# Performance work log

Measured on AMD Instinct MI355X. Metric: run time of the kernel, lower is better.

The kernel has to match this reference:

```python
import jax, jax.numpy as jnp
import numpy as np

TOPK = 6
ROUTE_SCALE = 1.5


def setup_inputs() -> dict:
    key = jax.random.key(0)
    k1, k2, k3 = jax.random.split(key, 3)
    N, D, E = 16384, 4096, 256
    x = jax.random.normal(k1, (N, D), dtype=jnp.float32)
    weight = jax.random.normal(k2, (E, D), dtype=jnp.float32) * (D ** -0.5)
    bias = jax.random.normal(k3, (E,), dtype=jnp.float32) * 0.02
    return {"x": x, "weight": weight, "bias": bias}


def reference(x, weight, bias):
    # gate linear: [N, D] @ [E, D]^T -> [N, E], computed in fp32
    scores = jnp.einsum('nd,ed->ne', x.astype(jnp.float32), weight.astype(jnp.float32))
    # sqrtsoftplus score function
    original_scores = jnp.sqrt(jax.nn.softplus(scores))
    # bias only affects expert selection, not the routing weights
    biased = original_scores + bias
    _, indices = jax.lax.top_k(biased, TOPK)          # [N, TOPK] int32
    weights = jnp.take_along_axis(original_scores, indices, axis=-1)
    # non-softmax score func -> renormalize selected weights
    weights = weights / jnp.sum(weights, axis=-1, keepdims=True)
    weights = weights * ROUTE_SCALE
    return weights, indices
```

## Files before the change

### kernel.cpp

```cpp
#include <hip/hip_runtime.h>
#include <math.h>

constexpr int D     = 4096;
constexpr int D4    = 1024;
constexpr int E     = 256;
constexpr int TK    = 6;
constexpr int BM    = 64;
constexpr int NT    = 512;
constexpr int NTILE = 128;
constexpr float TAU = 3e-5f;

typedef __attribute__((ext_vector_type(8)))  short short8;
typedef __attribute__((ext_vector_type(16))) float float16;
typedef unsigned short ushort_t;

#define GAS __attribute__((address_space(1)))
#define LAS __attribute__((address_space(3)))

__device__ __forceinline__ ushort_t f2bf(float f) {
  unsigned u = __float_as_uint(f);
  return (ushort_t)((u + 0x7fffu + ((u >> 16) & 1u)) >> 16);
}
__device__ __forceinline__ float bf2f(ushort_t h) {
  return __uint_as_float(((unsigned)h) << 16);
}
__device__ __forceinline__ int swz4(int r) { return (r & 3) ^ ((r >> 2) & 3); }

__device__ __forceinline__ void gload_lds16(const ushort_t* g, ushort_t* l) {
  __builtin_amdgcn_global_load_lds((const GAS unsigned int*)g,
                                   (LAS unsigned int*)l, 16, 0, 0);
}

struct __align__(16) SMem {
  union {
    struct {
      ushort_t Bh[4][8][32 * 32];
      ushort_t Bl[4][8][32 * 32];
      ushort_t Ah[2][BM * 32];
      ushort_t Al[2][BM * 32];
    } st;
    struct {
      float val[BM * 65];
      int   id [BM * 65];
    } mg;
  } u;
  float  bias[E];
  int    nflag;
  int    flagrow[BM];
  int    flagid[BM][8];
  double exact[8];
};
static_assert(sizeof(SMem) <= 160 * 1024, "LDS overflow");

__global__ __launch_bounds__(256)
void conv_w(const float* __restrict__ wg, ushort_t* __restrict__ whi,
            ushort_t* __restrict__ wlo)
{
  size_t i = (size_t)blockIdx.x * 256 + threadIdx.x;
  float4 v = ((const float4*)wg)[i];
  float a[4] = {v.x, v.y, v.z, v.w};
  ushort_t h[4], l[4];
#pragma unroll
  for (int j = 0; j < 4; ++j) {
    h[j] = f2bf(a[j]);
    l[j] = f2bf(a[j] - bf2f(h[j]));
  }
  *(uint2*)&whi[i * 4] = *(uint2*)h;
  *(uint2*)&wlo[i * 4] = *(uint2*)l;
}

#define WAITV5   asm volatile("s_waitcnt vmcnt(5)" ::: "memory")
#define WAITV0   asm volatile("s_waitcnt vmcnt(0)" ::: "memory")
#define LGKM0    asm volatile("s_waitcnt lgkmcnt(0)" ::: "memory")
#define MEMFENCE asm volatile("" ::: "memory")

__global__ __launch_bounds__(NT, 2)
void gate_kernel(const float* __restrict__ xg, const float* __restrict__ wg,
                 const float* __restrict__ bg,
                 const ushort_t* __restrict__ whi, const ushort_t* __restrict__ wlo,
                 float* __restrict__ outw, float* __restrict__ outi)
{
  __shared__ SMem sm;
  const int t    = threadIdx.x;
  const int row0 = blockIdx.x * BM;
  const int wv   = t >> 6;
  const int lane = t & 63;
  const int m    = lane & 31;
  const int hf   = lane >> 5;

  if (t < E) sm.bias[t] = bg[t];
  if (t == 0) sm.nflag = 0;

  const float4* x4 = (const float4*)xg;
  const float4* w4 = (const float4*)wg;

  float16 acc0, acc1;
#pragma unroll
  for (int i = 0; i < 16; ++i) { acc0[i] = 0.f; acc1[i] = 0.f; }

  const int a_row = t >> 3;
  const int a_c   = t & 7;

  const int e16 = lane >> 2;
  const int ch  = lane & 3;

  const int sA = swz4(m);

  auto stage_B = [&](int kt, int p) {
#pragma unroll
    for (int j = 0; j < 2; ++j) {
      const int er = j * 16 + e16;
      const int cs = ch ^ swz4(er);
      const size_t go = (size_t)(wv * 32 + er) * D + kt * 32 + cs * 8;
      gload_lds16(whi + go, &sm.u.st.Bh[p][wv][j * 512]);
      gload_lds16(wlo + go, &sm.u.st.Bl[p][wv][j * 512]);
    }
  };
  auto store_A = [&](int p, float4 xv) {
    float av[4] = {xv.x, xv.y, xv.z, xv.w};
    ushort_t h[4], l[4];
#pragma unroll
    for (int i = 0; i < 4; ++i) {
      h[i] = f2bf(av[i]);
      l[i] = f2bf(av[i] - bf2f(h[i]));
    }
    const int c  = a_c >> 1, hh = a_c & 1;
    const int sl = (c ^ swz4(a_row)) * 8 + hh * 4;
    *(uint2*)&sm.u.st.Ah[p][a_row * 32 + sl] = *(uint2*)h;
    *(uint2*)&sm.u.st.Al[p][a_row * 32 + sl] = *(uint2*)l;
  };
  auto compute = [&](int pa, int pb) {
#pragma unroll
    for (int ks = 0; ks < 2; ++ks) {
      const int sl = ((2 * ks + hf) ^ sA) * 8;
      short8 a0h = *(const short8*)&sm.u.st.Ah[pa][m * 32 + sl];
      short8 a0l = *(const short8*)&sm.u.st.Al[pa][m * 32 + sl];
      short8 a1h = *(const short8*)&sm.u.st.Ah[pa][(32 + m) * 32 + sl];
      short8 a1l = *(const short8*)&sm.u.st.Al[pa][(32 + m) * 32 + sl];
      short8 bh  = *(const short8*)&sm.u.st.Bh[pb][wv][m * 32 + sl];
      short8 bl  = *(const short8*)&sm.u.st.Bl[pb][wv][m * 32 + sl];
      acc0 = __builtin_amdgcn_mfma_f32_32x32x16_bf16(a0h, bh, acc0, 0, 0, 0);
      acc0 = __builtin_amdgcn_mfma_f32_32x32x16_bf16(a0h, bl, acc0, 0, 0, 0);
      acc0 = __builtin_amdgcn_mfma_f32_32x32x16_bf16(a0l, bh, acc0, 0, 0, 0);
      acc1 = __builtin_amdgcn_mfma_f32_32x32x16_bf16(a1h, bh, acc1, 0, 0, 0);
      acc1 = __builtin_amdgcn_mfma_f32_32x32x16_bf16(a1h, bl, acc1, 0, 0, 0);
      acc1 = __builtin_amdgcn_mfma_f32_32x32x16_bf16(a1l, bh, acc1, 0, 0, 0);
    }
  };

  float4 x0 = x4[(size_t)(row0 + a_row) * D4 + 0 * 8 + a_c];
  float4 xA = x4[(size_t)(row0 + a_row) * D4 + 1 * 8 + a_c];
  stage_B(0, 0);
  WAITV5;
  store_A(0, x0);
  float4 xB = x4[(size_t)(row0 + a_row) * D4 + 2 * 8 + a_c];
  stage_B(1, 1);
  LGKM0;
  __builtin_amdgcn_s_barrier();
  MEMFENCE;

#define TILE_BODY(KT, XS)                                                     \
  do {                                                                        \
    const int P   = (KT) & 3;                                                 \
    const int PW  = ((KT) + 2) & 3;                                           \
    const int PA  = (KT) & 1;                                                 \
    const int PA1 = ((KT) + 1) & 1;                                           \
    WAITV5;                                  \
    store_A(PA1, XS);                                                         \
    { const int kl = ((KT) + 3 < NTILE) ? (KT) + 3 : NTILE - 1;               \
      XS = x4[(size_t)(row0 + a_row) * D4 + kl * 8 + a_c]; }                  \
    { const int kb = ((KT) + 2 < NTILE) ? (KT) + 2 : NTILE - 1;               \
      stage_B(kb, PW); }                                                      \
    compute(PA, P);                                                           \
    LGKM0;                          \
    __builtin_amdgcn_s_barrier();                                             \
    MEMFENCE;                                                                 \
  } while (0)

  for (int it = 0; it < NTILE / 4; ++it) {
    const int kt = it * 4;
    TILE_BODY(kt + 0, xA);
    TILE_BODY(kt + 1, xB);
    TILE_BODY(kt + 2, xA);
    TILE_BODY(kt + 3, xB);
  }
#undef TILE_BODY

  WAITV0;
  __syncthreads();

  const int eBase  = wv * 32;
  const int myE    = eBase + m;
  const float myBias = sm.bias[myE];

#pragma unroll
  for (int b = 0; b < 2; ++b) {
#pragma unroll
    for (int reg = 0; reg < 16; ++reg) {
      const int row_local = b * 32 + (reg & 3) + 8 * (reg >> 2) + 4 * hf;
      float s = b ? acc1[reg] : acc0[reg];
      float v = sqrtf(fmaxf(s, 0.f) + log1pf(expf(-fabsf(s)))) + myBias;
#pragma unroll
      for (int ssel = 0; ssel < 8; ++ssel) {
        float bv = v;
#pragma unroll
        for (int off = 1; off < 32; off <<= 1)
          bv = fmaxf(bv, __shfl_xor(bv, off, 64));
        unsigned long long ball = __ballot(v == bv);
        unsigned hm = (unsigned)(ball >> (hf * 32));
        int mwin = __ffs(hm) - 1;
        if (m == mwin) {
          sm.u.mg.val[row_local * 65 + wv * 8 + ssel] = v;
          sm.u.mg.id [row_local * 65 + wv * 8 + ssel] = myE;
          v = -INFINITY;
        }
      }
    }
  }
  __syncthreads();

  {
    const int r = t >> 3, g = t & 7;
    float mv[8]; int mi[8];
#pragma unroll
    for (int q = 0; q < 8; ++q) {
      mv[q] = sm.u.mg.val[r * 65 + q * 8 + g];
      mi[q] = sm.u.mg.id [r * 65 + q * 8 + g];
    }
    float tv[8]; int ti[8];
#pragma unroll
    for (int s = 0; s < 8; ++s) {
      float bv = mv[0]; int bi = mi[0];
#pragma unroll
      for (int q = 1; q < 8; ++q)
        if (mv[q] > bv || (mv[q] == bv && mi[q] < bi)) { bv = mv[q]; bi = mi[q]; }
#pragma unroll
      for (int off = 1; off < 8; off <<= 1) {
        float ov = __shfl_xor(bv, off, 64);
        int   oi = __shfl_xor(bi, off, 64);
        if (ov > bv || (ov == bv && oi < bi)) { bv = ov; bi = oi; }
      }
      tv[s] = bv; ti[s] = bi;
#pragma unroll
      for (int q = 0; q < 8; ++q)
        if (mi[q] == bi) mv[q] = -INFINITY;
    }
    if (g == 0) {
      bool flag = false;
#pragma unroll
      for (int i = 0; i < 7; ++i) flag |= (tv[i] - tv[i + 1] < TAU);
      const int grow = row0 + r;
      if (!flag) {
        float og[6], ssum = 0.f;
#pragma unroll
        for (int i = 0; i < 6; ++i) { og[i] = tv[i] - sm.bias[ti[i]]; ssum += og[i]; }
        const float sc = 1.5f / ssum;
#pragma unroll
        for (int i = 0; i < 6; ++i) {
          outw[(size_t)grow * TK + i] = og[i] * sc;
          outi[(size_t)grow * TK + i] = (float)ti[i];
        }
      } else {
        int slot = atomicAdd(&sm.nflag, 1);
        sm.flagrow[slot] = grow;
#pragma unroll
        for (int i = 0; i < 8; ++i) sm.flagid[slot][i] = ti[i];
      }
    }
  }
  __syncthreads();

  const int nf = sm.nflag;
  for (int f = 0; f < nf; ++f) {
    const int grow = sm.flagrow[f];
    const int e    = sm.flagid[f][wv];
    double accd = 0.0;
    const float4* xr = x4 + (size_t)grow * D4 + lane * 16;
    const float4* wr = w4 + (size_t)e    * D4 + lane * 16;
#pragma unroll
    for (int i = 0; i < 16; ++i) {
      float4 xv = xr[i], wl = wr[i];
      accd = fma((double)xv.x, (double)wl.x, accd);
      accd = fma((double)xv.y, (double)wl.y, accd);
      accd = fma((double)xv.z, (double)wl.z, accd);
      accd = fma((double)xv.w, (double)wl.w, accd);
    }
#pragma unroll
    for (int off = 1; off < 64; off <<= 1)
      accd += __shfl_xor(accd, off, 64);
    if (lane == 0) {
      double sp = fmax(accd, 0.0) + log1p(exp(-fabs(accd)));
      sm.exact[wv] = sqrt(sp);
    }
    __syncthreads();
    if (t == 0) {
      double ov[8]; int oid[8], ordr[8];
      for (int i = 0; i < 8; ++i) { ov[i] = sm.exact[i]; oid[i] = sm.flagid[f][i]; ordr[i] = i; }
      for (int i = 0; i < 6; ++i) {
        int b = i;
        for (int j = i + 1; j < 8; ++j) {
          double bj = ov[ordr[j]] + (double)sm.bias[oid[ordr[j]]];
          double bb = ov[ordr[b]] + (double)sm.bias[oid[ordr[b]]];
          if (bj > bb || (bj == bb && oid[ordr[j]] < oid[ordr[b]])) b = j;
        }
        int tmp = ordr[i]; ordr[i] = ordr[b]; ordr[b] = tmp;
      }
      double ssum = 0.0;
      for (int i = 0; i < 6; ++i) ssum += ov[ordr[i]];
      double sc = 1.5 / ssum;
      for (int i = 0; i < 6; ++i) {
        outw[(size_t)grow * TK + i] = (float)(ov[ordr[i]] * sc);
        outi[(size_t)grow * TK + i] = (float)oid[ordr[i]];
      }
    }
    __syncthreads();
  }
}

extern "C" void kernel_launch(void* const* d_in, const int* in_sizes, int n_in,
                              void* d_out, int out_size, void* d_ws, size_t ws_size,
                              hipStream_t stream) {
  const float* x = (const float*)d_in[0];
  const float* w = (const float*)d_in[1];
  const float* b = (const float*)d_in[2];
  float* out  = (float*)d_out;
  const int N = in_sizes[0] / D;

  ushort_t* whi = (ushort_t*)d_ws;
  ushort_t* wlo = whi + (size_t)E * D;

  float* outw = out;
  float* outi = out + (size_t)N * TK;

  hipLaunchKernelGGL(conv_w, dim3(E * D / 4 / 256), dim3(256), 0, stream,
                     w, whi, wlo);
  hipLaunchKernelGGL(gate_kernel, dim3(N / BM), dim3(NT), 0, stream,
                     x, w, b, whi, wlo, outw, outi);
}
```

Before: 561.8 us.

## Split K across wave pairs with 1024-thread blocks and LDS reduction

Doubles the block to 16 waves. Each pair of waves shares one 32-expert slice and splits the K dimension of each 32-wide tile, one wave per half, instead of one wave walking the full tile. Each wave now stages only the hi or lo weight plane, and loads x as float2 to match the new thread count. Partial accumulators are summed through an LDS reduction buffer before the unchanged top-k epilogue, which runs on half of the waves. The aim is more waves in flight per CU to hide latency, at the cost of extra LDS traffic, a reduction step, idle waves in the epilogue, and stricter register limits from launch_bounds(1024,4).

```diff
diff --git a/kernel.cpp b/kernel.cpp
--- a/kernel.cpp
+++ b/kernel.cpp
@@ -2,11 +2,12 @@
 #include <math.h>
 
 constexpr int D     = 4096;
+constexpr int D2    = 2048;
 constexpr int D4    = 1024;
 constexpr int E     = 256;
 constexpr int TK    = 6;
 constexpr int BM    = 64;
-constexpr int NT    = 512;
+constexpr int NT    = 1024;
 constexpr int NTILE = 128;
 constexpr float TAU = 3e-5f;
 
@@ -40,9 +41,10 @@
       ushort_t Al[2][BM * 32];
     } st;
     struct {
+      float red[8][2][16][64];
       float val[BM * 65];
       int   id [BM * 65];
-    } mg;
+    } ep;
   } u;
   float  bias[E];
   int    nflag;
@@ -69,12 +71,13 @@
   *(uint2*)&wlo[i * 4] = *(uint2*)l;
 }
 
-#define WAITV5   asm volatile("s_waitcnt vmcnt(5)" ::: "memory")
+#define WAITV3   asm volatile("s_waitcnt vmcnt(3)" ::: "memory")
+#define WAITV2   asm volatile("s_waitcnt vmcnt(2)" ::: "memory")
 #define WAITV0   asm volatile("s_waitcnt vmcnt(0)" ::: "memory")
 #define LGKM0    asm volatile("s_waitcnt lgkmcnt(0)" ::: "memory")
 #define MEMFENCE asm volatile("" ::: "memory")
 
-__global__ __launch_bounds__(NT, 2)
+__global__ __launch_bounds__(NT, 4)
 void gate_kernel(const float* __restrict__ xg, const float* __restrict__ wg,
                  const float* __restrict__ bg,
                  const ushort_t* __restrict__ whi, const ushort_t* __restrict__ wlo,
@@ -87,10 +90,13 @@
   const int lane = t & 63;
   const int m    = lane & 31;
   const int hf   = lane >> 5;
+  const int eg   = wv >> 1;
+  const int kh   = wv & 1;
 
   if (t < E) sm.bias[t] = bg[t];
   if (t == 0) sm.nflag = 0;
 
+  const float2* x2 = (const float2*)xg;
   const float4* x4 = (const float4*)xg;
   const float4* w4 = (const float4*)wg;
 
@@ -98,81 +104,76 @@
 #pragma unroll
   for (int i = 0; i < 16; ++i) { acc0[i] = 0.f; acc1[i] = 0.f; }
 
-  const int a_row = t >> 3;
-  const int a_c   = t & 7;
+  const int a_row = t >> 4;
+  const int aq    = t & 15;
 
   const int e16 = lane >> 2;
   const int ch  = lane & 3;
 
   const int sA = swz4(m);
+  const int slR = ((2 * kh + hf) ^ sA) * 8;
+
+  const ushort_t* wsrc = kh ? wlo : whi;
 
   auto stage_B = [&](int kt, int p) {
+    ushort_t* dstbase = kh ? &sm.u.st.Bl[p][eg][0] : &sm.u.st.Bh[p][eg][0];
 #pragma unroll
     for (int j = 0; j < 2; ++j) {
       const int er = j * 16 + e16;
       const int cs = ch ^ swz4(er);
-      const size_t go = (size_t)(wv * 32 + er) * D + kt * 32 + cs * 8;
-      gload_lds16(whi + go, &sm.u.st.Bh[p][wv][j * 512]);
-      gload_lds16(wlo + go, &sm.u.st.Bl[p][wv][j * 512]);
+      const size_t go = (size_t)(eg * 32 + er) * D + kt * 32 + cs * 8;
+      gload_lds16(wsrc + go, dstbase + j * 512);
     }
   };
-  auto store_A = [&](int p, float4 xv) {
-    float av[4] = {xv.x, xv.y, xv.z, xv.w};
-    ushort_t h[4], l[4];
-#pragma unroll
-    for (int i = 0; i < 4; ++i) {
-      h[i] = f2bf(av[i]);
-      l[i] = f2bf(av[i] - bf2f(h[i]));
-    }
-    const int c  = a_c >> 1, hh = a_c & 1;
-    const int sl = (c ^ swz4(a_row)) * 8 + hh * 4;
-    *(uint2*)&sm.u.st.Ah[p][a_row * 32 + sl] = *(uint2*)h;
-    *(uint2*)&sm.u.st.Al[p][a_row * 32 + sl] = *(uint2*)l;
+  auto ldx = [&](int kt) {
+    return x2[(size_t)(row0 + a_row) * D2 + kt * 16 + aq];
+  };
+  auto store_A = [&](int p, float2 xv) {
+    ushort_t h0 = f2bf(xv.x), h1 = f2bf(xv.y);
+    ushort_t l0 = f2bf(xv.x - bf2f(h0)), l1 = f2bf(xv.y - bf2f(h1));
+    const int c = aq >> 2, sub = aq & 3;
+    const int sl = ((c ^ swz4(a_row)) << 3) + sub * 2;
+    unsigned hp = (unsigned)h0 | ((unsigned)h1 << 16);
+    unsigned lp = (unsigned)l0 | ((unsigned)l1 << 16);
+    *(unsigned*)&sm.u.st.Ah[p][a_row * 32 + sl] = hp;
+    *(unsigned*)&sm.u.st.Al[p][a_row * 32 + sl] = lp;
   };
   auto compute = [&](int pa, int pb) {
-#pragma unroll
-    for (int ks = 0; ks < 2; ++ks) {
-      const int sl = ((2 * ks + hf) ^ sA) * 8;
-      short8 a0h = *(const short8*)&sm.u.st.Ah[pa][m * 32 + sl];
-      short8 a0l = *(const short8*)&sm.u.st.Al[pa][m * 32 + sl];
-      short8 a1h = *(const short8*)&sm.u.st.Ah[pa][(32 + m) * 32 + sl];
-      short8 a1l = *(const short8*)&sm.u.st.Al[pa][(32 + m) * 32 + sl];
-      short8 bh  = *(const short8*)&sm.u.st.Bh[pb][wv][m * 32 + sl];
-      short8 bl  = *(const short8*)&sm.u.st.Bl[pb][wv][m * 32 + sl];
-      acc0 = __builtin_amdgcn_mfma_f32_32x32x16_bf16(a0h, bh, acc0, 0, 0, 0);
-      acc0 = __builtin_amdgcn_mfma_f32_32x32x16_bf16(a0h, bl, acc0, 0, 0, 0);
-      acc0 = __builtin_amdgcn_mfma_f32_32x32x16_bf16(a0l, bh, acc0, 0, 0, 0);
-      acc1 = __builtin_amdgcn_mfma_f32_32x32x16_bf16(a1h, bh, acc1, 0, 0, 0);
-      acc1 = __builtin_amdgcn_mfma_f32_32x32x16_bf16(a1h, bl, acc1, 0, 0, 0);
-      acc1 = __builtin_amdgcn_mfma_f32_32x32x16_bf16(a1l, bh, acc1, 0, 0, 0);
-    }
+    short8 a0h = *(const short8*)&sm.u.st.Ah[pa][m * 32 + slR];
+    short8 a0l = *(const short8*)&sm.u.st.Al[pa][m * 32 + slR];
+    short8 a1h = *(const short8*)&sm.u.st.Ah[pa][(32 + m) * 32 + slR];
+    short8 a1l = *(const short8*)&sm.u.st.Al[pa][(32 + m) * 32 + slR];
+    short8 bh  = *(const short8*)&sm.u.st.Bh[pb][eg][m * 32 + slR];
+    short8 bl  = *(const short8*)&sm.u.st.Bl[pb][eg][m * 32 + slR];
+    acc0 = __builtin_amdgcn_mfma_f32_32x32x16_bf16(a0h, bh, acc0, 0, 0, 0);
+    acc0 = __builtin_amdgcn_mfma_f32_32x32x16_bf16(a0h, bl, acc0, 0, 0, 0);
+    acc0 = __builtin_amdgcn_mfma_f32_32x32x16_bf16(a0l, bh, acc0, 0, 0, 0);
+    acc1 = __builtin_amdgcn_mfma_f32_32x32x16_bf16(a1h, bh, acc1, 0, 0, 0);
+    acc1 = __builtin_amdgcn_mfma_f32_32x32x16_bf16(a1h, bl, acc1, 0, 0, 0);
+    acc1 = __builtin_amdgcn_mfma_f32_32x32x16_bf16(a1l, bh, acc1, 0, 0, 0);
   };
 
-  float4 x0 = x4[(size_t)(row0 + a_row) * D4 + 0 * 8 + a_c];
-  float4 xA = x4[(size_t)(row0 + a_row) * D4 + 1 * 8 + a_c];
   stage_B(0, 0);
-  WAITV5;
-  store_A(0, x0);
-  float4 xB = x4[(size_t)(row0 + a_row) * D4 + 2 * 8 + a_c];
   stage_B(1, 1);
+  float2 x0v = ldx(0);
+  float2 xA  = ldx(1);
+  float2 xB  = ldx(2);
+  WAITV2;
+  store_A(0, x0v);
   LGKM0;
   __builtin_amdgcn_s_barrier();
   MEMFENCE;
 
 #define TILE_BODY(KT, XS)                                                     \
   do {                                                                        \
-    const int P   = (KT) & 3;                                                 \
-    const int PW  = ((KT) + 2) & 3;                                           \
-    const int PA  = (KT) & 1;                                                 \
-    const int PA1 = ((KT) + 1) & 1;                                           \
-    WAITV5;                                  \
-    store_A(PA1, XS);                                                         \
+    store_A(((KT) + 1) & 1, XS);                                              \
     { const int kl = ((KT) + 3 < NTILE) ? (KT) + 3 : NTILE - 1;               \
-      XS = x4[(size_t)(row0 + a_row) * D4 + kl * 8 + a_c]; }                  \
+      XS = ldx(kl); }                                                         \
     { const int kb = ((KT) + 2 < NTILE) ? (KT) + 2 : NTILE - 1;               \
-      stage_B(kb, PW); }                                                      \
-    compute(PA, P);                                                           \
-    LGKM0;                          \
+      stage_B(kb, ((KT) + 2) & 3); }                                          \
+    compute((KT) & 1, (KT) & 3);                                              \
+    WAITV3;                                      \
+    LGKM0;                                              \
     __builtin_amdgcn_s_barrier();                                             \
     MEMFENCE;                                                                 \
   } while (0)
@@ -189,43 +190,60 @@
   WAITV0;
   __syncthreads();
 
-  const int eBase  = wv * 32;
-  const int myE    = eBase + m;
+  if (kh == 1) {
+#pragma unroll
+    for (int r = 0; r < 16; ++r) {
+      sm.u.ep.red[eg][0][r][lane] = acc0[r];
+      sm.u.ep.red[eg][1][r][lane] = acc1[r];
+    }
+  }
+  __syncthreads();
+  if (kh == 0) {
+#pragma unroll
+    for (int r = 0; r < 16; ++r) {
+      acc0[r] += sm.u.ep.red[eg][0][r][lane];
+      acc1[r] += sm.u.ep.red[eg][1][r][lane];
+    }
+  }
+
+  const int myE = eg * 32 + m;
   const float myBias = sm.bias[myE];
 
-#pragma unroll
-  for (int b = 0; b < 2; ++b) {
-#pragma unroll
-    for (int reg = 0; reg < 16; ++reg) {
-      const int row_local = b * 32 + (reg & 3) + 8 * (reg >> 2) + 4 * hf;
-      float s = b ? acc1[reg] : acc0[reg];
-      float v = sqrtf(fmaxf(s, 0.f) + log1pf(expf(-fabsf(s)))) + myBias;
-#pragma unroll
-      for (int ssel = 0; ssel < 8; ++ssel) {
-        float bv = v;
-#pragma unroll
-        for (int off = 1; off < 32; off <<= 1)
-          bv = fmaxf(bv, __shfl_xor(bv, off, 64));
-        unsigned long long ball = __ballot(v == bv);
-        unsigned hm = (unsigned)(ball >> (hf * 32));
-        int mwin = __ffs(hm) - 1;
-        if (m == mwin) {
-          sm.u.mg.val[row_local * 65 + wv * 8 + ssel] = v;
-          sm.u.mg.id [row_local * 65 + wv * 8 + ssel] = myE;
-          v = -INFINITY;
+  if (kh == 0) {
+#pragma unroll
+    for (int b = 0; b < 2; ++b) {
+#pragma unroll
+      for (int reg = 0; reg < 16; ++reg) {
+        const int row_local = b * 32 + (reg & 3) + 8 * (reg >> 2) + 4 * hf;
+        float s = b ? acc1[reg] : acc0[reg];
+        float v = sqrtf(fmaxf(s, 0.f) + log1pf(expf(-fabsf(s)))) + myBias;
+#pragma unroll
+        for (int ssel = 0; ssel < 8; ++ssel) {
+          float bv = v;
+#pragma unroll
+          for (int off = 1; off < 32; off <<= 1)
+            bv = fmaxf(bv, __shfl_xor(bv, off, 64));
+          unsigned long long ball = __ballot(v == bv);
+          unsigned hm = (unsigned)(ball >> (hf * 32));
+          int mwin = __ffs(hm) - 1;
+          if (m == mwin) {
+            sm.u.ep.val[row_local * 65 + eg * 8 + ssel] = v;
+            sm.u.ep.id [row_local * 65 + eg * 8 + ssel] = myE;
+            v = -INFINITY;
+          }
         }
       }
     }
   }
   __syncthreads();
 
-  {
+  if (t < 512) {
     const int r = t >> 3, g = t & 7;
     float mv[8]; int mi[8];
 #pragma unroll
     for (int q = 0; q < 8; ++q) {
-      mv[q] = sm.u.mg.val[r * 65 + q * 8 + g];
-      mi[q] = sm.u.mg.id [r * 65 + q * 8 + g];
+      mv[q] = sm.u.ep.val[r * 65 + q * 8 + g];
+      mi[q] = sm.u.ep.id [r * 65 + q * 8 + g];
     }
     float tv[8]; int ti[8];
 #pragma unroll
@@ -273,24 +291,26 @@
   const int nf = sm.nflag;
   for (int f = 0; f < nf; ++f) {
     const int grow = sm.flagrow[f];
-    const int e    = sm.flagid[f][wv];
-    double accd = 0.0;
-    const float4* xr = x4 + (size_t)grow * D4 + lane * 16;
-    const float4* wr = w4 + (size_t)e    * D4 + lane * 16;
-#pragma unroll
-    for (int i = 0; i < 16; ++i) {
-      float4 xv = xr[i], wl = wr[i];
-      accd = fma((double)xv.x, (double)wl.x, accd);
-      accd = fma((double)xv.y, (double)wl.y, accd);
-      accd = fma((double)xv.z, (double)wl.z, accd);
-      accd = fma((double)xv.w, (double)wl.w, accd);
-    }
-#pragma unroll
-    for (int off = 1; off < 64; off <<= 1)
-      accd += __shfl_xor(accd, off, 64);
-    if (lane == 0) {
-      double sp = fmax(accd, 0.0) + log1p(exp(-fabs(accd)));
-      sm.exact[wv] = sqrt(sp);
+    if (wv < 8) {
+      const int e = sm.flagid[f][wv];
+      double accd = 0.0;
+      const float4* xr = x4 + (size_t)grow * D4 + lane * 16;
+      const float4* wr = w4 + (size_t)e    * D4 + lane * 16;
+#pragma unroll
+      for (int i = 0; i < 16; ++i) {
+        float4 xv = xr[i], wl = wr[i];
+        accd = fma((double)xv.x, (double)wl.x, accd);
+        accd = fma((double)xv.y, (double)wl.y, accd);
+        accd = fma((double)xv.z, (double)wl.z, accd);
+        accd = fma((double)xv.w, (double)wl.w, accd);
+      }
+#pragma unroll
+      for (int off = 1; off < 64; off <<= 1)
+        accd += __shfl_xor(accd, off, 64);
+      if (lane == 0) {
+        double sp = fmax(accd, 0.0) + log1p(exp(-fabs(accd)));
+        sm.exact[wv] = sqrt(sp);
+      }
     }
     __syncthreads();
     if (t == 0) {
```

Result: slower. 586.4 us (+4.4%).
